# Optimization experiments

Hardware: AMD Instinct MI355X
Metric: run time of the kernel (lower is better)

Reference implementation:

```python
import jax, jax.numpy as jnp
import numpy as np

SEQ, B, IN, H = 512, 256, 300, 256

def setup_inputs() -> dict:
    key = jax.random.key(0)
    ks = jax.random.split(key, 14)
    s = lambda *sh: 1.0 / np.sqrt(sh[0])
    inp = {
        'secuencia': jax.random.normal(ks[0], (SEQ, B, IN), jnp.float32),
        # RNN cell 1 (forward direction)
        'W1x': jax.random.normal(ks[1], (IN, H), jnp.float32) * s(IN),
        'W1h': jax.random.normal(ks[2], (H, H), jnp.float32) * s(H),
        'b1':  jax.random.normal(ks[3], (H,), jnp.float32) * 0.01,
        # RNN cell 2 (backward direction)
        'W2x': jax.random.normal(ks[4], (IN, H), jnp.float32) * s(IN),
        'W2h': jax.random.normal(ks[5], (H, H), jnp.float32) * s(H),
        'b2':  jax.random.normal(ks[6], (H,), jnp.float32) * 0.01,
        # MLP head (weights stored [in, out])
        'fc1_w': jax.random.normal(ks[7], (2 * H, 2 * H), jnp.float32) * s(2 * H),
        'fc1_b': jnp.zeros((2 * H,), jnp.float32),
        'fc2_w': jax.random.normal(ks[8], (2 * H, H), jnp.float32) * s(2 * H),
        'fc2_b': jnp.zeros((H,), jnp.float32),
        'fs_w':  jax.random.normal(ks[9], (H, 1), jnp.float32) * s(H),
        'fs_b':  jnp.zeros((1,), jnp.float32),
    }
    return inp

def _rnn_scan(seq, Wx, Wh, b):
    # seq: [S, B, IN] -> final hidden [B, H]; Elman cell h' = tanh(x Wx + h Wh + b)
    h0 = jnp.zeros((seq.shape[1], Wh.shape[0]), seq.dtype)
    def step(h, x):
        return jnp.tanh(x @ Wx + h @ Wh + b), None
    h_final, _ = jax.lax.scan(step, h0, seq)
    return h_final

def reference(secuencia, W1x, W1h, b1, W2x, W2h, b2,
              fc1_w, fc1_b, fc2_w, fc2_b, fs_w, fs_b):
    h1 = _rnn_scan(secuencia, W1x, W1h, b1)          # forward pass over time
    h2 = _rnn_scan(secuencia[::-1], W2x, W2h, b2)    # reversed pass over time
    h = jnp.concatenate([h1, h2], axis=1)            # [B, 2H]
    x = jax.nn.relu(h @ fc1_w + fc1_b)
    x = jax.nn.relu(x @ fc2_w + fc2_b)
    out = jnp.tanh(x @ fs_w + fs_b)                  # [B, 1]
    return out.squeeze()
```

## Files before the change

### kernel.cpp

```cpp
#include <hip/hip_runtime.h>

#define DI __device__ __forceinline__

typedef float f32x4 __attribute__((ext_vector_type(4)));
typedef float f4    __attribute__((ext_vector_type(4)));
typedef float f2    __attribute__((ext_vector_type(2)));
typedef _Float16 h8 __attribute__((ext_vector_type(8)));
typedef _Float16 h4 __attribute__((ext_vector_type(4)));

#define SEQL 512
#define BATCH 256
#define INF 300
#define HID 256
#define N2 512
#define KP 320
#define RNN_BLOCKS 32
#define GEMM_BLOCKS 2048


DI float ftanh(float x) {
    float e = __builtin_amdgcn_exp2f(x * 2.8853900817779268f);
    return fmaf(-2.0f, __builtin_amdgcn_rcpf(e + 1.0f), 1.0f);
}

DI h4 ald8(const void* p) {
    unsigned long long u = __hip_atomic_load((const unsigned long long*)p,
                                             __ATOMIC_RELAXED, __HIP_MEMORY_SCOPE_AGENT);
    union { unsigned long long u; h4 h; } c; c.u = u; return c.h;
}

__global__ void prep_kernel(const float* __restrict__ W1x, const float* __restrict__ W2x,
                            const float* __restrict__ b1, const float* __restrict__ b2,
                            _Float16* __restrict__ WTs, float* __restrict__ bcat,
                            unsigned* __restrict__ flags)
{
    int idx = blockIdx.x * 256 + threadIdx.x;
    if (idx < N2 * KP) {
        int j = idx / KP, z = idx - j * KP;
        int k = z ^ ((j & 7) << 3);
        float v = 0.f;
        if (k < INF) v = (j < HID) ? W1x[k * HID + j] : W2x[k * HID + (j - HID)];
        WTs[j * KP + z] = (_Float16)v;
    }
    if (idx < N2) bcat[idx] = (idx < HID) ? b1[idx] : b2[idx - HID];
    if (idx < 514) flags[idx] = (idx == 0 || idx == 513) ? 4u : 0u;
}

DI void fused_body(char* smem,
    const float* __restrict__ x, const _Float16* __restrict__ WTs,
    const float* __restrict__ bcat,
    const float* __restrict__ W1h, const float* __restrict__ W2h,
    _Float16* __restrict__ pre3, float* __restrict__ hcat,
    unsigned* __restrict__ flags)
{
    unsigned* flagb = flags + 1;
    const int tid = threadIdx.x;
    const int w = tid >> 6, l = tid & 63;
    const int lj = l & 15, lg = l >> 4;

    if (blockIdx.x >= RNN_BLOCKS) {
        _Float16* Ab = (_Float16*)smem;
        _Float16* Bb = (_Float16*)(smem + 16384);
        const int g = blockIdx.x - RNN_BLOCKS;
        const int k4i = g >> 2, r = g & 3;
        const int t = (k4i & 1) ? (511 - (k4i >> 1)) : (k4i >> 1);
        const int bm = 2 * t + (r >> 1);
        const int jn = r & 1;
        const size_t m0 = (size_t)bm * 128;
        const int j0b = jn * 256;
        const int wj = (w >> 1) * 64, wm2 = (w & 1) * 64;

        f32x4 acc[4][4];
#pragma unroll
        for (int a = 0; a < 4; ++a)
#pragma unroll
            for (int b = 0; b < 4; ++b) acc[a][b] = f32x4{0.f, 0.f, 0.f, 0.f};

        char* AbC = (char*)Ab;
        char* BbC = (char*)Bb;

        for (int s = 0; s < 5; ++s) {
            const int k0 = s * 64;
#pragma unroll
            for (int q = 0; q < 4; ++q) {
                int idx = q * 512 + tid;
                int jr = idx >> 3, sl = idx & 7;
                const _Float16* src = WTs + (size_t)(j0b + jr) * KP + k0 + sl * 8;
                _Float16* dst = &Bb[(q * 512 + w * 64) * 8];
                __builtin_amdgcn_global_load_lds(
                    (const __attribute__((address_space(1))) void*)src,
                    (__attribute__((address_space(3))) void*)dst, 16, 0, 0);
            }
#pragma unroll
            for (int c = 0; c < 4; ++c) {
                int f = c * 512 + tid;
                int mr = f >> 4, kq = f & 15;
                f4 v;
                if (k0 + kq * 4 + 3 < INF)
                    v = *(const f4*)(x + (m0 + mr) * INF + k0 + kq * 4);
                else
                    v = f4{0.f, 0.f, 0.f, 0.f};
                unsigned bo = (unsigned)mr * 128 + (((unsigned)kq * 8) ^ ((mr & 7) << 4));
                *(h4*)(AbC + bo) = h4{(_Float16)v[0], (_Float16)v[1], (_Float16)v[2], (_Float16)v[3]};
            }
            __syncthreads();
#pragma unroll
            for (int kk = 0; kk < 2; ++kk) {
                h8 aw[4], bx[4];
#pragma unroll
                for (int jt = 0; jt < 4; ++jt) {
                    int jr = wj + jt * 16 + lj;
                    unsigned bo = (unsigned)jr * 128 + (((unsigned)(kk * 64 + lg * 16)) ^ ((jr & 7) << 4));
                    aw[jt] = *(const h8*)(BbC + bo);
                }
#pragma unroll
                for (int mt = 0; mt < 4; ++mt) {
                    int mr = wm2 + mt * 16 + lj;
                    unsigned bo = (unsigned)mr * 128 + (((unsigned)(kk * 64 + lg * 16)) ^ ((mr & 7) << 4));
                    bx[mt] = *(const h8*)(AbC + bo);
                }
#pragma unroll
                for (int jt = 0; jt < 4; ++jt)
#pragma unroll
                    for (int mt = 0; mt < 4; ++mt)
                        acc[jt][mt] = __builtin_amdgcn_mfma_f32_16x16x32_f16(aw[jt], bx[mt], acc[jt][mt], 0, 0, 0);
            }
            __syncthreads();
        }
        f4 bias4[4];
#pragma unroll
        for (int jt = 0; jt < 4; ++jt)
            bias4[jt] = *(const f4*)(bcat + j0b + wj + jt * 16 + lg * 4);
        char* prc = (char*)pre3;
#pragma unroll
        for (int jt = 0; jt < 4; ++jt) {
            int slab = (j0b + wj + jt * 16) >> 4;
#pragma unroll
            for (int mt = 0; mt < 4; ++mt) {
                int M = (int)m0 + wm2 + mt * 16;
                size_t byte = (size_t)(M >> 8) * 262144 + (size_t)slab * 8192
                            + (size_t)((M & 255) + lj) * 32 + (size_t)lg * 8;
                h4 o;
#pragma unroll
                for (int i = 0; i < 4; ++i)
                    o[i] = (_Float16)(acc[jt][mt][i] + bias4[jt][i]);
                *(h4*)(prc + byte) = o;
            }
        }
        __syncthreads();
        if (tid == 0)
            __hip_atomic_fetch_add(&flagb[t], 1u, __ATOMIC_RELEASE, __HIP_MEMORY_SCOPE_AGENT);
        return;
    }

    __builtin_amdgcn_s_setprio(2);
    char* hbc = smem;
    const int dir = blockIdx.x & 1;
    const int b0 = (int)(blockIdx.x >> 1) * 16;
    const float* Wh = dir ? W2h : W1h;
    const int j0 = w * 32;
    const int dirOff = dir ? HID : 0;

    h8 afrag[2][8];
#pragma unroll
    for (int jt = 0; jt < 2; ++jt) {
        int jc = j0 + jt * 16 + lj;
#pragma unroll
        for (int kk = 0; kk < 8; ++kk) {
            h8 tr;
#pragma unroll
            for (int i = 0; i < 8; ++i) tr[i] = (_Float16)Wh[(kk * 32 + lg * 8 + i) * HID + jc];
            afrag[jt][kk] = tr;
        }
    }

    const unsigned rb = (unsigned)l * 16;
    const unsigned wb0 = (unsigned)w * 1024 + (unsigned)(lg >> 1) * 256
                       + (unsigned)lj * 16 + (unsigned)(lg & 1) * 8;

    ((h8*)hbc)[tid] = h8{0, 0, 0, 0, 0, 0, 0, 0};
    __syncthreads();

    const int fstep = dir ? -1 : 1;
    if (tid == 0) {
        unsigned* f0 = flagb + (dir ? 511 : 0);
#pragma unroll
        for (int i = 0; i < 3; ++i) {
            unsigned* f = f0 + i * fstep;
            while (__hip_atomic_load(f, __ATOMIC_ACQUIRE, __HIP_MEMORY_SCOPE_AGENT) < 4u)
                __builtin_amdgcn_s_sleep(2);
        }
    }
    __syncthreads();
    unsigned* fp = flagb + (dir ? 508 : 3);

    const long long sb = dir ? -262144LL : 262144LL;
    const char* pp = (const char*)pre3 + (long long)(dir ? (SEQL - 1) : 0) * 262144
                   + (long long)dir * 131072
                   + (long long)w * 16384 + (long long)(b0 + lj) * 32 + lg * 8;
    h4 pA[2], pB[2];
    pA[0] = ald8(pp); pA[1] = ald8(pp + 8192); pp += sb;
    pB[0] = ald8(pp); pB[1] = ald8(pp + 8192); pp += sb;

#define RNN_STEP(RB, WB, P, DO_PF)                                                    \
    do {                                                                              \
        h8 bf[8];                                                                     \
        _Pragma("unroll")                                                             \
        for (int kk = 0; kk < 8; ++kk)                                                \
            bf[kk] = *(const h8*)(hbc + (RB) + kk * 1024 + rb);                       \
        f32x4 acc0, acc1;                                                             \
        _Pragma("unroll")                                                             \
        for (int i = 0; i < 4; ++i) { acc0[i] = (float)P[0][i]; acc1[i] = (float)P[1][i]; } \
        if (DO_PF) {                                                                  \
            P[0] = ald8(pp);                                                          \
            P[1] = ald8(pp + 8192);                                                   \
            pp += sb;                                                                 \
        }                                                                             \
        _Pragma("unroll")                                                             \
        for (int kk = 0; kk < 8; ++kk)                                                \
            acc0 = __builtin_amdgcn_mfma_f32_16x16x32_f16(afrag[0][kk], bf[kk], acc0, 0, 0, 0); \
        h4 o0;                                                                        \
        _Pragma("unroll")                                                             \
        for (int i = 0; i < 4; ++i) o0[i] = (_Float16)ftanh(acc0[i]);                 \
        *(h4*)(hbc + (WB) + wb0) = o0;                                                \
        _Pragma("unroll")                                                             \
        for (int kk = 0; kk < 8; ++kk)                                                \
            acc1 = __builtin_amdgcn_mfma_f32_16x16x32_f16(afrag[1][kk], bf[kk], acc1, 0, 0, 0); \
        h4 o1;                                                                        \
        _Pragma("unroll")                                                             \
        for (int i = 0; i < 4; ++i) o1[i] = (_Float16)ftanh(acc1[i]);                 \
        *(h4*)(hbc + (WB) + wb0 + 512) = o1;                                          \
        if (DO_PF) {                                                                  \
            if (tid == 0) {                                                           \
                while (__hip_atomic_load(fp, __ATOMIC_ACQUIRE, __HIP_MEMORY_SCOPE_AGENT) < 4u) \
                    __builtin_amdgcn_s_sleep(2);                                      \
            }                                                                         \
            fp += fstep;                                                              \
        }                                                                             \
        __builtin_amdgcn_sched_barrier(0);                                            \
        asm volatile("s_waitcnt lgkmcnt(0)" ::: "memory");                            \
        __builtin_amdgcn_s_barrier();                                                 \
        __builtin_amdgcn_sched_barrier(0);                                            \
    } while (0)

    for (int tp = 0; tp < 255; ++tp) {
        RNN_STEP(0, 8192, pA, 1);
        RNN_STEP(8192, 0, pB, 1);
    }
    RNN_STEP(0, 8192, pA, 0);

    {
        f32x4 acc0, acc1;
#pragma unroll
        for (int i = 0; i < 4; ++i) { acc0[i] = (float)pB[0][i]; acc1[i] = (float)pB[1][i]; }
        h8 bf[8];
#pragma unroll
        for (int kk = 0; kk < 8; ++kk)
            bf[kk] = *(const h8*)(hbc + 8192 + kk * 1024 + rb);
#pragma unroll
        for (int kk = 0; kk < 8; ++kk) {
            acc0 = __builtin_amdgcn_mfma_f32_16x16x32_f16(afrag[0][kk], bf[kk], acc0, 0, 0, 0);
            acc1 = __builtin_amdgcn_mfma_f32_16x16x32_f16(afrag[1][kk], bf[kk], acc1, 0, 0, 0);
        }
        f4 v0, v1;
#pragma unroll
        for (int i = 0; i < 4; ++i) { v0[i] = ftanh(acc0[i]); v1[i] = ftanh(acc1[i]); }
        float* hc = hcat + (size_t)(b0 + lj) * N2 + dirOff + j0 + lg * 4;
        *(f4*)hc = v0;
        *(f4*)(hc + 16) = v1;
    }
#undef RNN_STEP
}

__global__ __launch_bounds__(512, 1) void fused_kernel_dyn(
    const float* __restrict__ x, const _Float16* __restrict__ WTs,
    const float* __restrict__ bcat,
    const float* __restrict__ W1h, const float* __restrict__ W2h,
    _Float16* __restrict__ pre3, float* __restrict__ hcat,
    unsigned* __restrict__ flags)
{
    extern __shared__ char smem[];
    fused_body(smem, x, WTs, bcat, W1h, W2h, pre3, hcat, flags);
}

__global__ __launch_bounds__(512, 2) void fused_kernel_sta(
    const float* __restrict__ x, const _Float16* __restrict__ WTs,
    const float* __restrict__ bcat,
    const float* __restrict__ W1h, const float* __restrict__ W2h,
    _Float16* __restrict__ pre3, float* __restrict__ hcat,
    unsigned* __restrict__ flags)
{
    __shared__ char smem[49152];
    fused_body(smem, x, WTs, bcat, W1h, W2h, pre3, hcat, flags);
}

__global__ __launch_bounds__(512) void head_mlp(
    const float* __restrict__ hcat,
    const float* __restrict__ fc1w, const float* __restrict__ fc1b,
    const float* __restrict__ fc2w, const float* __restrict__ fc2b,
    const float* __restrict__ fsw, const float* __restrict__ fsb,
    float* __restrict__ out)
{
    __shared__ float hs[4 * 512];
    __shared__ float y1[4 * 512];
    __shared__ float y2[4 * 256];
    __shared__ float red[8];
    const int tid = threadIdx.x;
    const int b0 = blockIdx.x * 4;
    const int r = tid >> 7;
    const int t = tid & 127;

    ((f4*)hs)[tid] = ((const f4*)(hcat + (size_t)b0 * N2))[tid];
    __syncthreads();

    {
        const int j0 = t * 4;
        f4 a = *(const f4*)(fc1b + j0);
#pragma unroll 4
        for (int k = 0; k < 512; ++k) {
            float h = hs[r * 512 + k];
            f4 w = *(const f4*)(fc1w + (size_t)k * 512 + j0);
#pragma unroll
            for (int i = 0; i < 4; ++i) a[i] = fmaf(h, w[i], a[i]);
        }
#pragma unroll
        for (int i = 0; i < 4; ++i) y1[r * 512 + j0 + i] = fmaxf(a[i], 0.f);
    }
    __syncthreads();

    {
        const int j2 = t * 2;
        f2 a = *(const f2*)(fc2b + j2);
#pragma unroll 4
        for (int k = 0; k < 512; ++k) {
            float yv = y1[r * 512 + k];
            f2 w = *(const f2*)(fc2w + (size_t)k * 256 + j2);
            a[0] = fmaf(yv, w[0], a[0]);
            a[1] = fmaf(yv, w[1], a[1]);
        }
        y2[r * 256 + j2]     = fmaxf(a[0], 0.f);
        y2[r * 256 + j2 + 1] = fmaxf(a[1], 0.f);
    }
    __syncthreads();

    {
        float p = fmaf(y2[r * 256 + t], fsw[t],
                       y2[r * 256 + 128 + t] * fsw[128 + t]);
#pragma unroll
        for (int off = 32; off > 0; off >>= 1) p += __shfl_down(p, off);
        if ((tid & 63) == 0) red[tid >> 6] = p;
    }
    __syncthreads();
    if (tid < 4) out[b0 + tid] = ftanh(red[2 * tid] + red[2 * tid + 1] + fsb[0]);
}

extern "C" void kernel_launch(void* const* d_in, const int* in_sizes, int n_in,
                              void* d_out, int out_size, void* d_ws, size_t ws_size,
                              hipStream_t stream)
{
    const float* x    = (const float*)d_in[0];
    const float* W1x  = (const float*)d_in[1];
    const float* W1h  = (const float*)d_in[2];
    const float* b1   = (const float*)d_in[3];
    const float* W2x  = (const float*)d_in[4];
    const float* W2h  = (const float*)d_in[5];
    const float* b2   = (const float*)d_in[6];
    const float* fc1w = (const float*)d_in[7];
    const float* fc1b = (const float*)d_in[8];
    const float* fc2w = (const float*)d_in[9];
    const float* fc2b = (const float*)d_in[10];
    const float* fsw  = (const float*)d_in[11];
    const float* fsb  = (const float*)d_in[12];

    char* ws = (char*)d_ws;
    size_t off = 0;
    _Float16* WTs   = (_Float16*)(ws + off); off += (size_t)N2 * KP * sizeof(_Float16);
    float* bcat     = (float*)(ws + off);    off += (size_t)N2 * sizeof(float);
    float* hcat     = (float*)(ws + off);    off += (size_t)BATCH * N2 * sizeof(float);
    unsigned* flags = (unsigned*)(ws + off); off += 4096;
    _Float16* pre3  = (_Float16*)(ws + off); off += (size_t)SEQL * BATCH * N2 * sizeof(_Float16);
    if (off > ws_size) return;

    prep_kernel<<<(N2 * KP + 255) / 256, 256, 0, stream>>>(W1x, W2x, b1, b2, WTs, bcat, flags);

    static hipError_t attr_err = hipFuncSetAttribute(
        (const void*)fused_kernel_dyn, hipFuncAttributeMaxDynamicSharedMemorySize, 81920);
    if (attr_err == hipSuccess) {
        fused_kernel_dyn<<<RNN_BLOCKS + GEMM_BLOCKS, 512, 81920, stream>>>(
            x, WTs, bcat, W1h, W2h, pre3, hcat, flags);
    } else {
        fused_kernel_sta<<<RNN_BLOCKS + GEMM_BLOCKS, 512, 0, stream>>>(
            x, WTs, bcat, W1h, W2h, pre3, hcat, flags);
    }
    head_mlp<<<64, 512, 0, stream>>>(hcat, fc1w, fc1b, fc2w, fc2b, fsw, fsb, (float*)d_out);
}
```

Before: 573.3 us.

## Coarsen producer/consumer flags to groups of eight timesteps; shrink MLP head block

Replaces per-timestep readiness flags with 64 group counters, each covering 8 timesteps (32 GEMM blocks). The RNN blocks now poll once every 8 steps, with every thread spinning, instead of thread 0 polling at each step. This cuts atomic polling and per-step spin overhead in the serial recurrence, but each group must fully finish before its 8 steps can start. The head MLP is also reworked to 256 threads, with each thread computing more outputs and one wave per batch row.

Measured after the change: 554.2 us. -3.3%, faster.

```diff
diff --git a/kernel.cpp b/kernel.cpp
--- a/kernel.cpp
+++ b/kernel.cpp
@@ -32,7 +32,7 @@
 __global__ void prep_kernel(const float* __restrict__ W1x, const float* __restrict__ W2x,
                             const float* __restrict__ b1, const float* __restrict__ b2,
                             _Float16* __restrict__ WTs, float* __restrict__ bcat,
-                            unsigned* __restrict__ flags)
+                            unsigned* __restrict__ gflags)
 {
     int idx = blockIdx.x * 256 + threadIdx.x;
     if (idx < N2 * KP) {
@@ -43,7 +43,7 @@
         WTs[j * KP + z] = (_Float16)v;
     }
     if (idx < N2) bcat[idx] = (idx < HID) ? b1[idx] : b2[idx - HID];
-    if (idx < 514) flags[idx] = (idx == 0 || idx == 513) ? 4u : 0u;
+    if (idx < 64) gflags[idx] = 0u;
 }
 
 DI void fused_body(char* smem,
@@ -51,9 +51,8 @@
     const float* __restrict__ bcat,
     const float* __restrict__ W1h, const float* __restrict__ W2h,
     _Float16* __restrict__ pre3, float* __restrict__ hcat,
-    unsigned* __restrict__ flags)
-{
-    unsigned* flagb = flags + 1;
+    unsigned* __restrict__ gflags)
+{
     const int tid = threadIdx.x;
     const int w = tid >> 6, l = tid & 63;
     const int lj = l & 15, lg = l >> 4;
@@ -149,7 +148,7 @@
         }
         __syncthreads();
         if (tid == 0)
-            __hip_atomic_fetch_add(&flagb[t], 1u, __ATOMIC_RELEASE, __HIP_MEMORY_SCOPE_AGENT);
+            __hip_atomic_fetch_add(&gflags[t >> 3], 1u, __ATOMIC_RELEASE, __HIP_MEMORY_SCOPE_AGENT);
         return;
     }
 
@@ -181,18 +180,14 @@
     ((h8*)hbc)[tid] = h8{0, 0, 0, 0, 0, 0, 0, 0};
     __syncthreads();
 
-    const int fstep = dir ? -1 : 1;
-    if (tid == 0) {
-        unsigned* f0 = flagb + (dir ? 511 : 0);
-#pragma unroll
-        for (int i = 0; i < 3; ++i) {
-            unsigned* f = f0 + i * fstep;
-            while (__hip_atomic_load(f, __ATOMIC_ACQUIRE, __HIP_MEMORY_SCOPE_AGENT) < 4u)
-                __builtin_amdgcn_s_sleep(2);
-        }
-    }
-    __syncthreads();
-    unsigned* fp = flagb + (dir ? 508 : 3);
+#define WAITG(G)                                                                      \
+    while (__hip_atomic_load(&gflags[(G)], __ATOMIC_ACQUIRE, __HIP_MEMORY_SCOPE_AGENT) < 32u) \
+        __builtin_amdgcn_s_sleep(8)
+
+    const int G0 = dir ? 63 : 0;
+    const int gstep = dir ? -1 : 1;
+    WAITG(G0);
+    WAITG(G0 + gstep);
 
     const long long sb = dir ? -262144LL : 262144LL;
     const char* pp = (const char*)pre3 + (long long)(dir ? (SEQL - 1) : 0) * 262144
@@ -230,25 +225,24 @@
         _Pragma("unroll")                                                             \
         for (int i = 0; i < 4; ++i) o1[i] = (_Float16)ftanh(acc1[i]);                 \
         *(h4*)(hbc + (WB) + wb0 + 512) = o1;                                          \
-        if (DO_PF) {                                                                  \
-            if (tid == 0) {                                                           \
-                while (__hip_atomic_load(fp, __ATOMIC_ACQUIRE, __HIP_MEMORY_SCOPE_AGENT) < 4u) \
-                    __builtin_amdgcn_s_sleep(2);                                      \
-            }                                                                         \
-            fp += fstep;                                                              \
-        }                                                                             \
         __builtin_amdgcn_sched_barrier(0);                                            \
         asm volatile("s_waitcnt lgkmcnt(0)" ::: "memory");                            \
         __builtin_amdgcn_s_barrier();                                                 \
         __builtin_amdgcn_sched_barrier(0);                                            \
     } while (0)
 
-    for (int tp = 0; tp < 255; ++tp) {
+    for (int i = 0; i < 63; ++i) {
+        if (i >= 1) { WAITG(G0 + (i + 1) * gstep); }
+        for (int p = 0; p < 4; ++p) {
+            RNN_STEP(0, 8192, pA, 1);
+            RNN_STEP(8192, 0, pB, 1);
+        }
+    }
+    for (int p = 0; p < 3; ++p) {
         RNN_STEP(0, 8192, pA, 1);
         RNN_STEP(8192, 0, pB, 1);
     }
     RNN_STEP(0, 8192, pA, 0);
-
     {
         f32x4 acc0, acc1;
 #pragma unroll
@@ -270,6 +264,7 @@
         *(f4*)(hc + 16) = v1;
     }
 #undef RNN_STEP
+#undef WAITG
 }
 
 __global__ __launch_bounds__(512, 1) void fused_kernel_dyn(
@@ -277,10 +272,10 @@
     const float* __restrict__ bcat,
     const float* __restrict__ W1h, const float* __restrict__ W2h,
     _Float16* __restrict__ pre3, float* __restrict__ hcat,
-    unsigned* __restrict__ flags)
+    unsigned* __restrict__ gflags)
 {
     extern __shared__ char smem[];
-    fused_body(smem, x, WTs, bcat, W1h, W2h, pre3, hcat, flags);
+    fused_body(smem, x, WTs, bcat, W1h, W2h, pre3, hcat, gflags);
 }
 
 __global__ __launch_bounds__(512, 2) void fused_kernel_sta(
@@ -288,13 +283,13 @@
     const float* __restrict__ bcat,
     const float* __restrict__ W1h, const float* __restrict__ W2h,
     _Float16* __restrict__ pre3, float* __restrict__ hcat,
-    unsigned* __restrict__ flags)
+    unsigned* __restrict__ gflags)
 {
     __shared__ char smem[49152];
-    fused_body(smem, x, WTs, bcat, W1h, W2h, pre3, hcat, flags);
-}
-
-__global__ __launch_bounds__(512) void head_mlp(
+    fused_body(smem, x, WTs, bcat, W1h, W2h, pre3, hcat, gflags);
+}
+
+__global__ __launch_bounds__(256) void head_mlp(
     const float* __restrict__ hcat,
     const float* __restrict__ fc1w, const float* __restrict__ fc1b,
     const float* __restrict__ fc2w, const float* __restrict__ fc2b,
@@ -304,54 +299,58 @@
     __shared__ float hs[4 * 512];
     __shared__ float y1[4 * 512];
     __shared__ float y2[4 * 256];
-    __shared__ float red[8];
     const int tid = threadIdx.x;
     const int b0 = blockIdx.x * 4;
-    const int r = tid >> 7;
-    const int t = tid & 127;
-
-    ((f4*)hs)[tid] = ((const f4*)(hcat + (size_t)b0 * N2))[tid];
+    const int r = tid >> 6;
+    const int lane = tid & 63;
+
+#pragma unroll
+    for (int c = 0; c < 2; ++c)
+        ((f4*)hs)[c * 256 + tid] = ((const f4*)(hcat + (size_t)b0 * N2))[c * 256 + tid];
     __syncthreads();
 
     {
-        const int j0 = t * 4;
-        f4 a = *(const f4*)(fc1b + j0);
-#pragma unroll 4
+        const int j0 = lane * 8;
+        f4 a0 = *(const f4*)(fc1b + j0);
+        f4 a1 = *(const f4*)(fc1b + j0 + 4);
         for (int k = 0; k < 512; ++k) {
             float h = hs[r * 512 + k];
-            f4 w = *(const f4*)(fc1w + (size_t)k * 512 + j0);
-#pragma unroll
-            for (int i = 0; i < 4; ++i) a[i] = fmaf(h, w[i], a[i]);
-        }
-#pragma unroll
-        for (int i = 0; i < 4; ++i) y1[r * 512 + j0 + i] = fmaxf(a[i], 0.f);
+            f4 w0 = *(const f4*)(fc1w + (size_t)k * 512 + j0);
+            f4 w1 = *(const f4*)(fc1w + (size_t)k * 512 + j0 + 4);
+#pragma unroll
+            for (int i = 0; i < 4; ++i) { a0[i] = fmaf(h, w0[i], a0[i]); a1[i] = fmaf(h, w1[i], a1[i]); }
+        }
+#pragma unroll
+        for (int i = 0; i < 4; ++i) {
+            y1[r * 512 + j0 + i]     = fmaxf(a0[i], 0.f);
+            y1[r * 512 + j0 + 4 + i] = fmaxf(a1[i], 0.f);
+        }
     }
     __syncthreads();
 
     {
-        const int j2 = t * 2;
-        f2 a = *(const f2*)(fc2b + j2);
-#pragma unroll 4
+        const int j2 = lane * 4;
+        f4 a = *(const f4*)(fc2b + j2);
         for (int k = 0; k < 512; ++k) {
             float yv = y1[r * 512 + k];
-            f2 w = *(const f2*)(fc2w + (size_t)k * 256 + j2);
-            a[0] = fmaf(yv, w[0], a[0]);
-            a[1] = fmaf(yv, w[1], a[1]);
-        }
-        y2[r * 256 + j2]     = fmaxf(a[0], 0.f);
-        y2[r * 256 + j2 + 1] = fmaxf(a[1], 0.f);
+            f4 w = *(const f4*)(fc2w + (size_t)k * 256 + j2);
+#pragma unroll
+            for (int i = 0; i < 4; ++i) a[i] = fmaf(yv, w[i], a[i]);
+        }
+#pragma unroll
+        for (int i = 0; i < 4; ++i) y2[r * 256 + j2 + i] = fmaxf(a[i], 0.f);
     }
     __syncthreads();
 
     {
-        float p = fmaf(y2[r * 256 + t], fsw[t],
-                       y2[r * 256 + 128 + t] * fsw[128 + t]);
+        float p = 0.f;
+#pragma unroll
+        for (int u = 0; u < 4; ++u)
+            p = fmaf(y2[r * 256 + lane + u * 64], fsw[lane + u * 64], p);
 #pragma unroll
         for (int off = 32; off > 0; off >>= 1) p += __shfl_down(p, off);
-        if ((tid & 63) == 0) red[tid >> 6] = p;
-    }
-    __syncthreads();
-    if (tid < 4) out[b0 + tid] = ftanh(red[2 * tid] + red[2 * tid + 1] + fsb[0]);
+        if (lane == 0) out[b0 + r] = ftanh(p + fsb[0]);
+    }
 }
 
 extern "C" void kernel_launch(void* const* d_in, const int* in_sizes, int n_in,
@@ -374,23 +373,23 @@
 
     char* ws = (char*)d_ws;
     size_t off = 0;
-    _Float16* WTs   = (_Float16*)(ws + off); off += (size_t)N2 * KP * sizeof(_Float16);
-    float* bcat     = (float*)(ws + off);    off += (size_t)N2 * sizeof(float);
-    float* hcat     = (float*)(ws + off);    off += (size_t)BATCH * N2 * sizeof(float);
-    unsigned* flags = (unsigned*)(ws + off); off += 4096;
-    _Float16* pre3  = (_Float16*)(ws + off); off += (size_t)SEQL * BATCH * N2 * sizeof(_Float16);
+    _Float16* WTs    = (_Float16*)(ws + off); off += (size_t)N2 * KP * sizeof(_Float16);
+    float* bcat      = (float*)(ws + off);    off += (size_t)N2 * sizeof(float);
+    float* hcat      = (float*)(ws + off);    off += (size_t)BATCH * N2 * sizeof(float);
+    unsigned* gflags = (unsigned*)(ws + off); off += 4096;
+    _Float16* pre3   = (_Float16*)(ws + off); off += (size_t)SEQL * BATCH * N2 * sizeof(_Float16);
     if (off > ws_size) return;
 
-    prep_kernel<<<(N2 * KP + 255) / 256, 256, 0, stream>>>(W1x, W2x, b1, b2, WTs, bcat, flags);
+    prep_kernel<<<(N2 * KP + 255) / 256, 256, 0, stream>>>(W1x, W2x, b1, b2, WTs, bcat, gflags);
 
     static hipError_t attr_err = hipFuncSetAttribute(
         (const void*)fused_kernel_dyn, hipFuncAttributeMaxDynamicSharedMemorySize, 81920);
     if (attr_err == hipSuccess) {
         fused_kernel_dyn<<<RNN_BLOCKS + GEMM_BLOCKS, 512, 81920, stream>>>(
-            x, WTs, bcat, W1h, W2h, pre3, hcat, flags);
+            x, WTs, bcat, W1h, W2h, pre3, hcat, gflags);
     } else {
         fused_kernel_sta<<<RNN_BLOCKS + GEMM_BLOCKS, 512, 0, stream>>>(
-            x, WTs, bcat, W1h, W2h, pre3, hcat, flags);
-    }
-    head_mlp<<<64, 512, 0, stream>>>(hcat, fc1w, fc1b, fc2w, fc2b, fsw, fsb, (float*)d_out);
-}
+            x, WTs, bcat, W1h, W2h, pre3, hcat, gflags);
+    }
+    head_mlp<<<64, 256, 0, stream>>>(hcat, fc1w, fc1b, fc2w, fc2b, fsw, fsb, (float*)d_out);
+}
```
